# Performance work log

Measured on AMD Instinct MI355X. Metric: run time of the kernel, lower is better.

Reference implementation:

```python
import jax, jax.numpy as jnp
import numpy as np

NUM_HEADS = 8
WEIGHTS_DIM = 512
INPUT_DIM = 512
D_HEAD = WEIGHTS_DIM // NUM_HEADS


def setup_inputs() -> dict:
    key = jax.random.key(0)
    ks = jax.random.split(key, 9)
    B, S, D = 4, 2048, INPUT_DIM
    s_in = 1.0 / np.sqrt(D)
    s_w = 1.0 / np.sqrt(WEIGHTS_DIM)
    return {
        "x": jax.random.normal(ks[0], (B, S, D), dtype=jnp.float32),
        "Wq": jax.random.normal(ks[1], (D, WEIGHTS_DIM), dtype=jnp.float32) * s_in,
        "bq": jnp.zeros((WEIGHTS_DIM,), dtype=jnp.float32),
        "Wk": jax.random.normal(ks[2], (D, WEIGHTS_DIM), dtype=jnp.float32) * s_in,
        "bk": jnp.zeros((WEIGHTS_DIM,), dtype=jnp.float32),
        "Wv": jax.random.normal(ks[3], (D, WEIGHTS_DIM), dtype=jnp.float32) * s_in,
        "bv": jnp.zeros((WEIGHTS_DIM,), dtype=jnp.float32),
        "Wh": jax.random.normal(ks[4], (WEIGHTS_DIM, D), dtype=jnp.float32) * s_w,
        "bh": jnp.zeros((D,), dtype=jnp.float32),
    }


def _split_heads(t):
    # [B, S, Dm] -> [B, H, S, d_head]
    B, S, _ = t.shape
    return t.reshape(B, S, NUM_HEADS, D_HEAD).transpose(0, 2, 1, 3)


def reference(x, Wq, bq, Wk, bk, Wv, bv, Wh, bh):
    q = _split_heads(x @ Wq + bq)
    k = _split_heads(x @ Wk + bk)
    v = _split_heads(x @ Wv + bv)
    scale = 1.0 / jnp.sqrt(jnp.float32(D_HEAD))
    scores = jnp.einsum("bhqd,bhkd->bhqk", q, k) * scale  # [B,H,S,S]
    weights = jax.nn.softmax(scores, axis=-1)
    attn = jnp.einsum("bhqk,bhkd->bhqd", weights, v)
    B, H, S, d = attn.shape
    concat = attn.transpose(0, 2, 1, 3).reshape(B, S, H * d)
    return concat @ Wh + bh
```

## Files before the change

### kernel.cpp

```cpp
#include <hip/hip_runtime.h>
#include <stdint.h>

#define NB  4
#define SS  2048
#define DD  512
#define HH  8
#define DHH 64
#define MM  (NB * SS)

typedef __attribute__((ext_vector_type(8))) short bf16x8;
typedef __attribute__((ext_vector_type(4))) float f32x4;
typedef __attribute__((ext_vector_type(4))) short s16x4;

union fu32 { float f; unsigned u; };

static __device__ __forceinline__ short f2bf(float f) {
  fu32 a; a.f = f;
  unsigned u = a.u;
  return (short)((u + 0x7fffu + ((u >> 16) & 1u)) >> 16);
}
static __device__ __forceinline__ float bf2f(short s) {
  fu32 t; t.u = ((unsigned)(unsigned short)s) << 16;
  return t.f;
}

static __device__ __forceinline__ void async16(const void* g, void* l) {
  __builtin_amdgcn_global_load_lds(
      (__attribute__((address_space(1))) unsigned*)(void*)g,
      (__attribute__((address_space(3))) unsigned*)l, 16, 0, 0);
}

__global__ __launch_bounds__(256) void prep_kernel(
    const float* __restrict__ x, short* __restrict__ xb,
    const float* __restrict__ W0, const float* __restrict__ W1,
    const float* __restrict__ W2, const float* __restrict__ W3,
    short* __restrict__ T0, short* __restrict__ T1,
    short* __restrict__ T2, short* __restrict__ T3) {
  const int bid = blockIdx.x, tid = threadIdx.x;
  if (bid < 2048) {
    int i = (bid * 256 + tid) * 8;
    float4 v0 = *(const float4*)(x + i);
    float4 v1 = *(const float4*)(x + i + 4);
    bf16x8 o;
    o[0] = f2bf(v0.x); o[1] = f2bf(v0.y); o[2] = f2bf(v0.z); o[3] = f2bf(v0.w);
    o[4] = f2bf(v1.x); o[5] = f2bf(v1.y); o[6] = f2bf(v1.z); o[7] = f2bf(v1.w);
    *(bf16x8*)(xb + i) = o;
  } else {
    int z = bid - 2048;
    int widx = z >> 6, rem = z & 63;
    const float* W = widx == 0 ? W0 : widx == 1 ? W1 : widx == 2 ? W2 : W3;
    short*       T = widx == 0 ? T0 : widx == 1 ? T1 : widx == 2 ? T2 : T3;
    int n  = (rem & 7) * 64 + (tid & 63);
    int k0 = (rem >> 3) * 64 + (tid >> 6) * 16;
    bf16x8 t0, t1;
#pragma unroll
    for (int j = 0; j < 8; ++j) t0[j] = f2bf(W[(size_t)(k0 + j) * DD + n]);
#pragma unroll
    for (int j = 0; j < 8; ++j) t1[j] = f2bf(W[(size_t)(k0 + 8 + j) * DD + n]);
    *(bf16x8*)(T + (size_t)n * DD + k0)     = t0;
    *(bf16x8*)(T + (size_t)n * DD + k0 + 8) = t1;
  }
}

__global__ __launch_bounds__(256, 3) void gemm_qkv_kernel(
    const short* __restrict__ A, const short* __restrict__ Bt,
    const float* __restrict__ bq, const float* __restrict__ bk,
    const float* __restrict__ bv, short* __restrict__ qout,
    short* __restrict__ kout, short* __restrict__ vtout, float qscale) {
  __shared__ __align__(16) short a_sh[128 * 64];
  __shared__ __align__(16) short b_sh[128 * 64];
  const int tid  = threadIdx.x;
  const int w    = tid >> 6, lane = tid & 63, quad = lane >> 4, l16 = lane & 15;
  const int m0   = blockIdx.y * 128, n0 = blockIdx.x * 128;
  const int m0w  = (w >> 1) * 64,    n0w = (w & 1) * 64;
  const int rw   = lane >> 3, seg = lane & 7, gs = seg ^ rw;
  const int sxz  = l16 & 7;

  f32x4 acc[4][4];
#pragma unroll
  for (int i = 0; i < 4; ++i)
#pragma unroll
    for (int j = 0; j < 4; ++j) acc[i][j] = {0.f, 0.f, 0.f, 0.f};

  for (int kt = 0; kt < DD; kt += 64) {
    __syncthreads();
    {
      const short* ga = A  + (size_t)(m0 + w * 32 + rw) * DD + kt + gs * 8;
      const short* gb = Bt + (size_t)(n0 + w * 32 + rw) * DD + kt + gs * 8;
#pragma unroll
      for (int i = 0; i < 4; ++i) {
        async16(ga + (size_t)i * 8 * DD, &a_sh[(w * 32 + i * 8) * 64]);
        async16(gb + (size_t)i * 8 * DD, &b_sh[(w * 32 + i * 8) * 64]);
      }
    }
    __syncthreads();
#pragma unroll
    for (int ks = 0; ks < 2; ++ks) {
      const int so = ((ks * 4 + quad) ^ sxz) * 8;
      bf16x8 af[4], bfr[4];
#pragma unroll
      for (int mt = 0; mt < 4; ++mt)
        af[mt] = *(const bf16x8*)&a_sh[(m0w + mt * 16 + l16) * 64 + so];
#pragma unroll
      for (int nt = 0; nt < 4; ++nt)
        bfr[nt] = *(const bf16x8*)&b_sh[(n0w + nt * 16 + l16) * 64 + so];
#pragma unroll
      for (int mt = 0; mt < 4; ++mt)
#pragma unroll
        for (int nt = 0; nt < 4; ++nt)
          acc[mt][nt] = __builtin_amdgcn_mfma_f32_16x16x32_bf16(
              af[mt], bfr[nt], acc[mt][nt], 0, 0, 0);
    }
  }

#pragma unroll
  for (int nt = 0; nt < 4; ++nt) {
    const int n   = n0 + n0w + nt * 16 + l16;
    const int sg  = n >> 9, n9 = n & 511, h = n9 >> 6, d = n & 63;
    const float bval = (sg == 0 ? bq : sg == 1 ? bk : bv)[n9];
    const float scl  = (sg == 0) ? qscale : 1.0f;
#pragma unroll
    for (int mt = 0; mt < 4; ++mt) {
      const int mb = m0 + m0w + mt * 16 + quad * 4;
      const int bi = mb >> 11, s = mb & (SS - 1);
      if (sg == 2) {
        s16x4 pk;
#pragma unroll
        for (int r = 0; r < 4; ++r) pk[r] = f2bf(acc[mt][nt][r] + bval);
        *(s16x4*)&vtout[((size_t)(bi * HH + h) * DHH + d) * SS + s] = pk;
      } else {
        short* o = (sg == 0) ? qout : kout;
        const size_t base = ((size_t)(bi * HH + h) * SS + s) * DHH + d;
#pragma unroll
        for (int r = 0; r < 4; ++r)
          o[base + (size_t)r * DHH] = f2bf((acc[mt][nt][r] + bval) * scl);
      }
    }
  }
}

__global__ __launch_bounds__(256, 3) void attn_kernel(
    const short* __restrict__ Qa, const short* __restrict__ Ka,
    const short* __restrict__ Vt, short* __restrict__ Op0,
    short* __restrict__ Op1, float* __restrict__ lpw) {
  __shared__ __align__(16) short k_sh[128 * 64];
  __shared__ __align__(16) short vt_sh[64 * 128];
  __shared__ __align__(16) short p_sh[4][32 * 68];

  const int tid  = threadIdx.x;
  const int w    = tid >> 6, lane = tid & 63, quad = lane >> 4, l16 = lane & 15;
  const int n    = blockIdx.x;
  const int grp  = (n & 7) * 8 + (n >> 7);
  const int qt_b = (n >> 3) & 15;
  const int half = grp & 1, h = (grp >> 1) & 7, b = grp >> 4;
  const int q0   = qt_b * 128;
  const int rw = lane >> 3, seg = lane & 7, gs = seg ^ rw;
  const int sxz = l16 & 7;
  const size_t base = (size_t)(b * HH + h) * SS * DHH;
  const short* Qg = Qa + base + (size_t)(q0 + w * 32) * DHH;
  const short* Kg = Ka + base;
  const short* Vg = Vt + base;

  bf16x8 qf[2][2];
#pragma unroll
  for (int mt = 0; mt < 2; ++mt)
#pragma unroll
    for (int ks = 0; ks < 2; ++ks)
      qf[mt][ks] = *(const bf16x8*)(Qg + (size_t)(mt * 16 + l16) * DHH + ks * 32 + quad * 8);

  f32x4 o_acc[2][4];
#pragma unroll
  for (int mt = 0; mt < 2; ++mt)
#pragma unroll
    for (int dt = 0; dt < 4; ++dt) o_acc[mt][dt] = {0.f, 0.f, 0.f, 0.f};
  float rsq[2] = {0.f, 0.f};

  short* pw = p_sh[w];
  const int kstart = half * (SS / 2);

  for (int kb = kstart; kb < kstart + SS / 2; kb += 128) {
    __syncthreads();
    {
      const short* gk = Kg + (size_t)(kb + w * 32 + rw) * DHH + gs * 8;
#pragma unroll
      for (int i = 0; i < 4; ++i)
        async16(gk + (size_t)i * 8 * DHH, &k_sh[(w * 32 + i * 8) * 64]);
#pragma unroll
      for (int i = 0; i < 4; ++i) {
        const int d = w * 16 + i * 4 + (lane >> 4);
        const int gseg = (lane & 15) ^ (d & 15);
        async16(Vg + (size_t)d * SS + kb + gseg * 8,
                &vt_sh[(w * 16 + i * 4) * 128]);
      }
    }
    __syncthreads();

    f32x4 st[2][8];
#pragma unroll
    for (int knt = 0; knt < 8; ++knt) {
      f32x4 s0 = {0.f, 0.f, 0.f, 0.f}, s1 = {0.f, 0.f, 0.f, 0.f};
#pragma unroll
      for (int ks = 0; ks < 2; ++ks) {
        bf16x8 kf = *(const bf16x8*)&k_sh[(knt * 16 + l16) * 64 + ((ks * 4 + quad) ^ sxz) * 8];
        s0 = __builtin_amdgcn_mfma_f32_16x16x32_bf16(kf, qf[0][ks], s0, 0, 0, 0);
        s1 = __builtin_amdgcn_mfma_f32_16x16x32_bf16(kf, qf[1][ks], s1, 0, 0, 0);
      }
      st[0][knt] = s0; st[1][knt] = s1;
    }

#pragma unroll
    for (int h64 = 0; h64 < 2; ++h64) {
#pragma unroll
      for (int qt = 0; qt < 2; ++qt)
#pragma unroll
        for (int kl = 0; kl < 4; ++kl) {
          f32x4 s = st[qt][h64 * 4 + kl];
          fu32 e0, e1, e2, e3;
          e0.f = exp2f(s[0]); e1.f = exp2f(s[1]);
          e2.f = exp2f(s[2]); e3.f = exp2f(s[3]);
          uint2 pk;
          pk.x = __builtin_amdgcn_perm(e1.u, e0.u, 0x07060302u);
          pk.y = __builtin_amdgcn_perm(e3.u, e2.u, 0x07060302u);
          *(uint2*)&pw[(qt * 16 + l16) * 68 + kl * 16 + quad * 4] = pk;
          fu32 t0, t1, t2, t3;
          t0.u = e0.u & 0xffff0000u; t1.u = e1.u & 0xffff0000u;
          t2.u = e2.u & 0xffff0000u; t3.u = e3.u & 0xffff0000u;
          rsq[qt] += (t0.f + t1.f) + (t2.f + t3.f);
        }
#pragma unroll
      for (int ck = 0; ck < 2; ++ck) {
        const int g = h64 * 8 + ck * 4 + quad;
        bf16x8 pf0 = *(const bf16x8*)&pw[l16 * 68 + ck * 32 + quad * 8];
        bf16x8 pf1 = *(const bf16x8*)&pw[(16 + l16) * 68 + ck * 32 + quad * 8];
#pragma unroll
        for (int dt = 0; dt < 4; ++dt) {
          bf16x8 vf = *(const bf16x8*)&vt_sh[(dt * 16 + l16) * 128 + (g ^ l16) * 8];
          o_acc[0][dt] = __builtin_amdgcn_mfma_f32_16x16x32_bf16(pf0, vf, o_acc[0][dt], 0, 0, 0);
          o_acc[1][dt] = __builtin_amdgcn_mfma_f32_16x16x32_bf16(pf1, vf, o_acc[1][dt], 0, 0, 0);
        }
      }
    }
  }

#pragma unroll
  for (int qt = 0; qt < 2; ++qt) {
    float v = rsq[qt];
    v += __shfl_xor(v, 16);
    v += __shfl_xor(v, 32);
    rsq[qt] = v;
  }

  short* Op = half ? Op1 : Op0;
#pragma unroll
  for (int qt = 0; qt < 2; ++qt) {
    if (quad == 0) {
      const int qg = q0 + w * 32 + qt * 16 + l16;
      lpw[(size_t)half * (NB * HH * SS) + (size_t)(b * HH + h) * SS + qg] = rsq[qt];
    }
#pragma unroll
    for (int r = 0; r < 4; ++r) {
      const float lv  = __shfl(rsq[qt], quad * 4 + r, 16);
      const float inv = 1.f / lv;
      const int qg = q0 + w * 32 + qt * 16 + quad * 4 + r;
      const size_t row = (size_t)(b * HH + h) * SS + qg;
#pragma unroll
      for (int dt = 0; dt < 4; ++dt)
        Op[row * DHH + dt * 16 + l16] = f2bf(o_acc[qt][dt][r] * inv);
    }
  }
}

__global__ void attn_combine_kernel(const short* __restrict__ Op0,
                                    const short* __restrict__ Op1,
                                    const float* __restrict__ lpw,
                                    short* __restrict__ aws) {
  int idx  = blockIdx.x * 256 + threadIdx.x;
  int dsg  = idx & 7;
  int row  = idx >> 3;
  int q    = row & (SS - 1);
  int bh   = row >> 11, h = bh & 7, b = bh >> 3;
  float l1 = lpw[row], l2 = lpw[NB * HH * SS + row];
  float inv = 1.f / (l1 + l2);
  float w1 = l1 * inv, w2 = l2 * inv;
  bf16x8 a = *(const bf16x8*)&Op0[(size_t)row * DHH + dsg * 8];
  bf16x8 c = *(const bf16x8*)&Op1[(size_t)row * DHH + dsg * 8];
  bf16x8 o;
#pragma unroll
  for (int j = 0; j < 8; ++j) o[j] = f2bf(w1 * bf2f(a[j]) + w2 * bf2f(c[j]));
  *(bf16x8*)&aws[((size_t)(b * SS + q)) * DD + h * DHH + dsg * 8] = o;
}

__global__ __launch_bounds__(256, 2) void gemm_proj_kernel(
    const short* __restrict__ A, const short* __restrict__ Bt,
    const float* __restrict__ bias, float* __restrict__ out) {
  __shared__ __align__(16) short a_sh[128 * 64];
  __shared__ __align__(16) short b_sh[64 * 64];
  const int tid = threadIdx.x;
  const int w   = tid >> 6, lane = tid & 63, quad = lane >> 4, l16 = lane & 15;
  const int m0  = blockIdx.y * 128, n0 = blockIdx.x * 64;
  const int m0w = w * 32;
  const int rw  = lane >> 3, seg = lane & 7, gs = seg ^ rw;
  const int sxz = l16 & 7;

  f32x4 acc[2][4];
#pragma unroll
  for (int i = 0; i < 2; ++i)
#pragma unroll
    for (int j = 0; j < 4; ++j) acc[i][j] = {0.f, 0.f, 0.f, 0.f};

  for (int kt = 0; kt < DD; kt += 64) {
    __syncthreads();
    {
      const short* ga = A  + (size_t)(m0 + w * 32 + rw) * DD + kt + gs * 8;
      const short* gb = Bt + (size_t)(n0 + w * 16 + rw) * DD + kt + gs * 8;
#pragma unroll
      for (int i = 0; i < 4; ++i)
        async16(ga + (size_t)i * 8 * DD, &a_sh[(w * 32 + i * 8) * 64]);
#pragma unroll
      for (int i = 0; i < 2; ++i)
        async16(gb + (size_t)i * 8 * DD, &b_sh[(w * 16 + i * 8) * 64]);
    }
    __syncthreads();
#pragma unroll
    for (int ks = 0; ks < 2; ++ks) {
      const int so = ((ks * 4 + quad) ^ sxz) * 8;
      bf16x8 af0 = *(const bf16x8*)&a_sh[(m0w + l16) * 64 + so];
      bf16x8 af1 = *(const bf16x8*)&a_sh[(m0w + 16 + l16) * 64 + so];
#pragma unroll
      for (int nt = 0; nt < 4; ++nt) {
        bf16x8 bfr = *(const bf16x8*)&b_sh[(nt * 16 + l16) * 64 + so];
        acc[0][nt] = __builtin_amdgcn_mfma_f32_16x16x32_bf16(af0, bfr, acc[0][nt], 0, 0, 0);
        acc[1][nt] = __builtin_amdgcn_mfma_f32_16x16x32_bf16(af1, bfr, acc[1][nt], 0, 0, 0);
      }
    }
  }

#pragma unroll
  for (int nt = 0; nt < 4; ++nt) {
    const int   n  = n0 + nt * 16 + l16;
    const float bv = bias[n];
#pragma unroll
    for (int mt = 0; mt < 2; ++mt)
#pragma unroll
      for (int r = 0; r < 4; ++r) {
        const int m = m0 + m0w + mt * 16 + quad * 4 + r;
        out[(size_t)m * DD + n] = acc[mt][nt][r] + bv;
      }
  }
}

extern "C" void kernel_launch(void* const* d_in, const int* in_sizes, int n_in,
                              void* d_out, int out_size, void* d_ws, size_t ws_size,
                              hipStream_t stream) {
  (void)in_sizes; (void)n_in; (void)out_size; (void)ws_size;
  const float* x  = (const float*)d_in[0];
  const float* Wq = (const float*)d_in[1];
  const float* bq = (const float*)d_in[2];
  const float* Wk = (const float*)d_in[3];
  const float* bk = (const float*)d_in[4];
  const float* Wv = (const float*)d_in[5];
  const float* bv = (const float*)d_in[6];
  const float* Wh = (const float*)d_in[7];
  const float* bh = (const float*)d_in[8];

  short* ws  = (short*)d_ws;
  short* xb  = ws;
  short* wqt = xb  + (size_t)MM * DD;
  short* wkt = wqt + (size_t)DD * DD;
  short* wvt = wkt + (size_t)DD * DD;
  short* wht = wvt + (size_t)DD * DD;
  short* qws = wht + (size_t)DD * DD;
  short* kws = qws + (size_t)MM * DD;
  short* vws = kws + (size_t)MM * DD;
  short* aws = vws + (size_t)MM * DD;
  short* op1 = aws + (size_t)MM * DD;
  float* lpw = (float*)(op1 + (size_t)MM * DD);

  hipLaunchKernelGGL(prep_kernel, dim3(2048 + 256), dim3(256), 0, stream,
                     x, xb, Wq, Wk, Wv, Wh, wqt, wkt, wvt, wht);

  const float qscale = 1.4426950408889634f / 8.0f;
  hipLaunchKernelGGL(gemm_qkv_kernel, dim3(12, 64), dim3(256), 0, stream,
                     xb, wqt, bq, bk, bv, qws, kws, vws, qscale);

  hipLaunchKernelGGL(attn_kernel, dim3(1024), dim3(256), 0, stream,
                     qws, kws, vws, xb, op1, lpw);
  hipLaunchKernelGGL(attn_combine_kernel, dim3(NB * HH * SS * 8 / 256), dim3(256), 0, stream,
                     xb, op1, lpw, aws);

  hipLaunchKernelGGL(gemm_proj_kernel, dim3(8, 64), dim3(256), 0, stream,
                     aws, wht, bh, (float*)d_out);
}
```

Baseline: 202.9 us.

## Keep softmax probabilities in registers via lane permutes and MFMA row sums

Removes the per-wave LDS staging buffer for the P tile. Probabilities are now rearranged into the MFMA A-operand layout in registers using shfl_xor and ds_bpermute. Row sums are computed with an extra MFMA against a ones vector instead of scalar adds and shuffles. Occupancy is raised to 4 blocks per SM, since shared memory and register pressure drop. The cost is extra permute instructions and one additional MFMA per chunk, plus a register cap that could cause spills.

```diff
diff --git a/kernel.cpp b/kernel.cpp
--- a/kernel.cpp
+++ b/kernel.cpp
@@ -13,6 +13,7 @@
 typedef __attribute__((ext_vector_type(4))) short s16x4;
 
 union fu32 { float f; unsigned u; };
+union pfu  { uint4 u; bf16x8 v; };
 
 static __device__ __forceinline__ short f2bf(float f) {
   fu32 a; a.f = f;
@@ -139,13 +140,12 @@
   }
 }
 
-__global__ __launch_bounds__(256, 3) void attn_kernel(
+__global__ __launch_bounds__(256, 4) void attn_kernel(
     const short* __restrict__ Qa, const short* __restrict__ Ka,
     const short* __restrict__ Vt, short* __restrict__ Op0,
     short* __restrict__ Op1, float* __restrict__ lpw) {
   __shared__ __align__(16) short k_sh[128 * 64];
   __shared__ __align__(16) short vt_sh[64 * 128];
-  __shared__ __align__(16) short p_sh[4][32 * 68];
 
   const int tid  = threadIdx.x;
   const int w    = tid >> 6, lane = tid & 63, quad = lane >> 4, l16 = lane & 15;
@@ -168,14 +168,21 @@
     for (int ks = 0; ks < 2; ++ks)
       qf[mt][ks] = *(const bf16x8*)(Qg + (size_t)(mt * 16 + l16) * DHH + ks * 32 + quad * 8);
 
+  bf16x8 ones;
+#pragma unroll
+  for (int j = 0; j < 8; ++j) ones[j] = (short)0x3F80;
+
   f32x4 o_acc[2][4];
 #pragma unroll
-  for (int mt = 0; mt < 2; ++mt)
-#pragma unroll
-    for (int dt = 0; dt < 4; ++dt) o_acc[mt][dt] = {0.f, 0.f, 0.f, 0.f};
-  float rsq[2] = {0.f, 0.f};
-
-  short* pw = p_sh[w];
+  for (int qt = 0; qt < 2; ++qt)
+#pragma unroll
+    for (int dt = 0; dt < 4; ++dt) o_acc[qt][dt] = {0.f, 0.f, 0.f, 0.f};
+  f32x4 l_acc[2] = {{0.f, 0.f, 0.f, 0.f}, {0.f, 0.f, 0.f, 0.f}};
+
+  const int addrA = ((((quad & 1) << 1) + (quad >> 1)) * 16 + l16) * 4;
+  const int addrB = addrA ^ 64;
+  const bool qeven = (quad & 1) == 0;
+
   const int kstart = half * (SS / 2);
 
   for (int kb = kstart; kb < kstart + SS / 2; kb += 128) {
@@ -195,74 +202,60 @@
     }
     __syncthreads();
 
-    f32x4 st[2][8];
-#pragma unroll
-    for (int knt = 0; knt < 8; ++knt) {
-      f32x4 s0 = {0.f, 0.f, 0.f, 0.f}, s1 = {0.f, 0.f, 0.f, 0.f};
-#pragma unroll
-      for (int ks = 0; ks < 2; ++ks) {
-        bf16x8 kf = *(const bf16x8*)&k_sh[(knt * 16 + l16) * 64 + ((ks * 4 + quad) ^ sxz) * 8];
-        s0 = __builtin_amdgcn_mfma_f32_16x16x32_bf16(kf, qf[0][ks], s0, 0, 0, 0);
-        s1 = __builtin_amdgcn_mfma_f32_16x16x32_bf16(kf, qf[1][ks], s1, 0, 0, 0);
-      }
-      st[0][knt] = s0; st[1][knt] = s1;
-    }
-
-#pragma unroll
-    for (int h64 = 0; h64 < 2; ++h64) {
-#pragma unroll
-      for (int qt = 0; qt < 2; ++qt)
-#pragma unroll
-        for (int kl = 0; kl < 4; ++kl) {
-          f32x4 s = st[qt][h64 * 4 + kl];
+#pragma unroll
+    for (int ck = 0; ck < 4; ++ck) {
+      uint2 pk[2][2];
+#pragma unroll
+      for (int t = 0; t < 2; ++t) {
+        const int knt = ck * 2 + t;
+        bf16x8 kf0 = *(const bf16x8*)&k_sh[(knt * 16 + l16) * 64 + ((0 * 4 + quad) ^ sxz) * 8];
+        bf16x8 kf1 = *(const bf16x8*)&k_sh[(knt * 16 + l16) * 64 + ((1 * 4 + quad) ^ sxz) * 8];
+#pragma unroll
+        for (int qt = 0; qt < 2; ++qt) {
+          f32x4 s = {0.f, 0.f, 0.f, 0.f};
+          s = __builtin_amdgcn_mfma_f32_16x16x32_bf16(kf0, qf[qt][0], s, 0, 0, 0);
+          s = __builtin_amdgcn_mfma_f32_16x16x32_bf16(kf1, qf[qt][1], s, 0, 0, 0);
           fu32 e0, e1, e2, e3;
           e0.f = exp2f(s[0]); e1.f = exp2f(s[1]);
           e2.f = exp2f(s[2]); e3.f = exp2f(s[3]);
-          uint2 pk;
-          pk.x = __builtin_amdgcn_perm(e1.u, e0.u, 0x07060302u);
-          pk.y = __builtin_amdgcn_perm(e3.u, e2.u, 0x07060302u);
-          *(uint2*)&pw[(qt * 16 + l16) * 68 + kl * 16 + quad * 4] = pk;
-          fu32 t0, t1, t2, t3;
-          t0.u = e0.u & 0xffff0000u; t1.u = e1.u & 0xffff0000u;
-          t2.u = e2.u & 0xffff0000u; t3.u = e3.u & 0xffff0000u;
-          rsq[qt] += (t0.f + t1.f) + (t2.f + t3.f);
+          pk[qt][t].x = __builtin_amdgcn_perm(e1.u, e0.u, 0x07060302u);
+          pk[qt][t].y = __builtin_amdgcn_perm(e3.u, e2.u, 0x07060302u);
         }
-#pragma unroll
-      for (int ck = 0; ck < 2; ++ck) {
-        const int g = h64 * 8 + ck * 4 + quad;
-        bf16x8 pf0 = *(const bf16x8*)&pw[l16 * 68 + ck * 32 + quad * 8];
-        bf16x8 pf1 = *(const bf16x8*)&pw[(16 + l16) * 68 + ck * 32 + quad * 8];
-#pragma unroll
-        for (int dt = 0; dt < 4; ++dt) {
-          bf16x8 vf = *(const bf16x8*)&vt_sh[(dt * 16 + l16) * 128 + (g ^ l16) * 8];
-          o_acc[0][dt] = __builtin_amdgcn_mfma_f32_16x16x32_bf16(pf0, vf, o_acc[0][dt], 0, 0, 0);
-          o_acc[1][dt] = __builtin_amdgcn_mfma_f32_16x16x32_bf16(pf1, vf, o_acc[1][dt], 0, 0, 0);
-        }
-      }
-    }
-  }
-
+      }
+      pfu pf[2];
+#pragma unroll
+      for (int qt = 0; qt < 2; ++qt) {
+        unsigned p1x = (unsigned)__shfl_xor((int)pk[qt][1].x, 16);
+        unsigned p1y = (unsigned)__shfl_xor((int)pk[qt][1].y, 16);
+        unsigned v0x = qeven ? pk[qt][0].x : p1x;
+        unsigned v0y = qeven ? pk[qt][0].y : p1y;
+        unsigned v2x = qeven ? p1x : pk[qt][0].x;
+        unsigned v2y = qeven ? p1y : pk[qt][0].y;
+        pf[qt].u.x = (unsigned)__builtin_amdgcn_ds_bpermute(addrA, (int)v0x);
+        pf[qt].u.y = (unsigned)__builtin_amdgcn_ds_bpermute(addrA, (int)v0y);
+        pf[qt].u.z = (unsigned)__builtin_amdgcn_ds_bpermute(addrB, (int)v2x);
+        pf[qt].u.w = (unsigned)__builtin_amdgcn_ds_bpermute(addrB, (int)v2y);
+        l_acc[qt] = __builtin_amdgcn_mfma_f32_16x16x32_bf16(pf[qt].v, ones, l_acc[qt], 0, 0, 0);
+      }
+#pragma unroll
+      for (int dt = 0; dt < 4; ++dt) {
+        bf16x8 vf = *(const bf16x8*)&vt_sh[(dt * 16 + l16) * 128 + ((ck * 4 + quad) ^ l16) * 8];
+        o_acc[0][dt] = __builtin_amdgcn_mfma_f32_16x16x32_bf16(pf[0].v, vf, o_acc[0][dt], 0, 0, 0);
+        o_acc[1][dt] = __builtin_amdgcn_mfma_f32_16x16x32_bf16(pf[1].v, vf, o_acc[1][dt], 0, 0, 0);
+      }
+    }
+  }
+
+  short* Op = half ? Op1 : Op0;
 #pragma unroll
   for (int qt = 0; qt < 2; ++qt) {
-    float v = rsq[qt];
-    v += __shfl_xor(v, 16);
-    v += __shfl_xor(v, 32);
-    rsq[qt] = v;
-  }
-
-  short* Op = half ? Op1 : Op0;
-#pragma unroll
-  for (int qt = 0; qt < 2; ++qt) {
-    if (quad == 0) {
-      const int qg = q0 + w * 32 + qt * 16 + l16;
-      lpw[(size_t)half * (NB * HH * SS) + (size_t)(b * HH + h) * SS + qg] = rsq[qt];
-    }
 #pragma unroll
     for (int r = 0; r < 4; ++r) {
-      const float lv  = __shfl(rsq[qt], quad * 4 + r, 16);
-      const float inv = 1.f / lv;
       const int qg = q0 + w * 32 + qt * 16 + quad * 4 + r;
       const size_t row = (size_t)(b * HH + h) * SS + qg;
+      if (l16 == 0)
+        lpw[(size_t)half * (NB * HH * SS) + row] = l_acc[qt][r];
+      const float inv = 1.f / l_acc[qt][r];
 #pragma unroll
       for (int dt = 0; dt < 4; ++dt)
         Op[row * DHH + dt * 16 + l16] = f2bf(o_acc[qt][dt][r] * inv);
```

New measurement: 190.9 us. 5.9% less time.
